# Kernel tuning notes

Hardware: AMD Instinct MI355X
Metric: run time of the kernel (lower is better)

Reference implementation:

```python
import jax, jax.numpy as jnp
import numpy as np

B, F, E = 16384, 50, 64

def setup_inputs() -> dict:
    key = jax.random.key(0)
    k1, k2, k3, k4 = jax.random.split(key, 4)
    g = jax.random.uniform(k1, (B, F, F), dtype=jnp.float32)
    h = jax.random.normal(k2, (B, F, E), dtype=jnp.float32)
    W_in = jax.random.normal(k3, (F, E, E), dtype=jnp.float32) * (2.0 / (E + E)) ** 0.5
    W_out = jax.random.normal(k4, (F, E, E), dtype=jnp.float32) * (2.0 / (E + E)) ** 0.5
    bias_p = jnp.zeros((E,), dtype=jnp.float32)
    return {"g": g, "h": h, "W_in": W_in, "W_out": W_out, "bias_p": bias_p}

def reference(g, h, W_in, W_out, bias_p):
    # per-field transform: [F,E,E] x [B,F,E] -> [B,F,E]
    h_out = jnp.einsum('fij,bfj->bfi', W_out, h)
    # graph aggregation over fields: [B,F,F] x [B,F,E] -> [B,F,E]
    aggr = jnp.einsum('bfg,bge->bfe', g, h_out)
    # per-field input transform + bias
    a = jnp.einsum('fij,bfj->bfi', W_in, aggr) + bias_p
    return a
```

## Files before the change

kernel.cpp:

```cpp
#include <hip/hip_runtime.h>


static constexpr int Bz  = 16384;
static constexpr int Ff  = 50;
static constexpr int Ee  = 64;
static constexpr int BT  = 128;
static constexpr int LDW = 68;

__device__ __forceinline__ void fma4(float4& a, float s, const float4& v) {
    a.x += s * v.x; a.y += s * v.y; a.z += s * v.z; a.w += s * v.w;
}

__global__ __launch_bounds__(128, 2)
void field_gemm(const float* __restrict__ src, float* __restrict__ dst,
                const float* __restrict__ W, const float* __restrict__ bias) {
    __shared__ float W_lds[Ee * LDW];
    __shared__ float h_lds[BT * LDW];
    const int f  = blockIdx.y;
    const int b0 = blockIdx.x * BT;
    const int t  = threadIdx.x;

    const float4* Wf4 = (const float4*)(W + f * Ee * Ee);
#pragma unroll
    for (int k = 0; k < 8; ++k) {
        int q = k * 128 + t;
        *(float4*)&W_lds[(q >> 4) * LDW + (q & 15) * 4] = Wf4[q];
    }
    const float4* s4 = (const float4*)src;
#pragma unroll
    for (int k = 0; k < 16; ++k) {
        int q = k * 128 + t;
        int r = q >> 4;
        *(float4*)&h_lds[r * LDW + (q & 15) * 4] =
            s4[(b0 + r) * (Ff * Ee / 4) + f * 16 + (q & 15)];
    }
    __syncthreads();

    const int ti = t & 7;
    const int tb = t >> 3;
    float acc[8][8];
#pragma unroll
    for (int ii = 0; ii < 8; ++ii)
#pragma unroll
        for (int kb = 0; kb < 8; ++kb) acc[ii][kb] = 0.f;

#pragma unroll 2
    for (int j0 = 0; j0 < Ee; j0 += 4) {
        float4 w4[8], h4[8];
#pragma unroll
        for (int ii = 0; ii < 8; ++ii)
            w4[ii] = *(const float4*)&W_lds[(ti + 8 * ii) * LDW + j0];
#pragma unroll
        for (int kb = 0; kb < 8; ++kb)
            h4[kb] = *(const float4*)&h_lds[(tb + 16 * kb) * LDW + j0];
#pragma unroll
        for (int ii = 0; ii < 8; ++ii)
#pragma unroll
            for (int kb = 0; kb < 8; ++kb) {
                acc[ii][kb] += w4[ii].x * h4[kb].x;
                acc[ii][kb] += w4[ii].y * h4[kb].y;
                acc[ii][kb] += w4[ii].z * h4[kb].z;
                acc[ii][kb] += w4[ii].w * h4[kb].w;
            }
    }

#pragma unroll
    for (int ii = 0; ii < 8; ++ii) {
        const int i  = ti + 8 * ii;
        const float bv = bias ? bias[i] : 0.0f;
#pragma unroll
        for (int kb = 0; kb < 8; ++kb) {
            const int bb = tb + 16 * kb;
            dst[(b0 + bb) * (Ff * Ee) + f * Ee + i] = acc[ii][kb] + bv;
        }
    }
}

static constexpr int HOP = 52 * Ee;
static constexpr int GPD = 2560;
static constexpr int WRG = HOP + GPD;

__global__ __launch_bounds__(128, 2)
void aggr_inplace(const float* __restrict__ g, float* __restrict__ ho) {
    __shared__ float lds[2 * WRG];
    const int t    = threadIdx.x;
    const int wid  = t >> 6;
    const int lane = t & 63;
    const int b    = blockIdx.x * 2 + wid;
    float* ho_sh = &lds[wid * WRG];
    float* g_sh  = ho_sh + HOP;

    const float4* hosrc = (const float4*)(ho + (size_t)b * (Ff * Ee));
    const float4* gsrc  = (const float4*)(g  + (size_t)b * (Ff * Ff));
#pragma unroll
    for (int k = 0; k < 13; ++k) {
        int q = k * 64 + lane;
        if (q < Ff * Ee / 4) *(float4*)&ho_sh[q * 4] = hosrc[q];
    }
#pragma unroll
    for (int k = 0; k < 10; ++k) {
        int q = k * 64 + lane;
        if (q < (Ff * Ff + 3) / 4) *(float4*)&g_sh[q * 4] = gsrc[q];
    }
    *(float2*)&ho_sh[Ff * Ee + lane * 2] = make_float2(0.f, 0.f);
    if (lane < 30) *(float2*)&g_sh[Ff * Ff + lane * 2] = make_float2(0.f, 0.f);
    __syncthreads();

    const int te = lane & 7;
    const int tf = lane >> 3;
    const int e0 = te * 8;
    float4 acc[7][2];
#pragma unroll
    for (int k = 0; k < 7; ++k) {
        acc[k][0] = make_float4(0.f, 0.f, 0.f, 0.f);
        acc[k][1] = make_float4(0.f, 0.f, 0.f, 0.f);
    }

#pragma unroll 2
    for (int g0 = 0; g0 < 52; g0 += 4) {
        float4 ho4[4][2];
#pragma unroll
        for (int q = 0; q < 4; ++q) {
            ho4[q][0] = *(const float4*)&ho_sh[(g0 + q) * Ee + e0];
            ho4[q][1] = *(const float4*)&ho_sh[(g0 + q) * Ee + e0 + 4];
        }
#pragma unroll
        for (int k = 0; k < 7; ++k) {
            int fi = tf * 7 + k;
            fi = (fi < Ff) ? fi : (Ff - 1);
            const float2 ga = *(const float2*)&g_sh[fi * Ff + g0];
            const float2 gb = *(const float2*)&g_sh[fi * Ff + g0 + 2];
            fma4(acc[k][0], ga.x, ho4[0][0]); fma4(acc[k][1], ga.x, ho4[0][1]);
            fma4(acc[k][0], ga.y, ho4[1][0]); fma4(acc[k][1], ga.y, ho4[1][1]);
            fma4(acc[k][0], gb.x, ho4[2][0]); fma4(acc[k][1], gb.x, ho4[2][1]);
            fma4(acc[k][0], gb.y, ho4[3][0]); fma4(acc[k][1], gb.y, ho4[3][1]);
        }
    }

    float* hb = ho + (size_t)b * (Ff * Ee);
#pragma unroll
    for (int k = 0; k < 7; ++k) {
        const int fi = tf * 7 + k;
        if (fi < Ff) {
            *(float4*)&hb[fi * Ee + e0]     = acc[k][0];
            *(float4*)&hb[fi * Ee + e0 + 4] = acc[k][1];
        }
    }
}

extern "C" void kernel_launch(void* const* d_in, const int* in_sizes, int n_in,
                              void* d_out, int out_size, void* d_ws, size_t ws_size,
                              hipStream_t stream) {
    const float* g     = (const float*)d_in[0];
    const float* h     = (const float*)d_in[1];
    const float* W_in  = (const float*)d_in[2];
    const float* W_out = (const float*)d_in[3];
    const float* bias  = (const float*)d_in[4];
    float* out = (float*)d_out;

    dim3 grid1(Bz / BT, Ff);
    field_gemm<<<grid1, 128, 0, stream>>>(h, out, W_out, nullptr);
    aggr_inplace<<<Bz / 2, 128, 0, stream>>>(g, out);
    field_gemm<<<grid1, 128, 0, stream>>>(out, out, W_in, bias);
}
```

Measured before the change: 674.8 us.

## Use direct global-to-LDS loads with XOR swizzle and larger batch tiles in field GEMM

The field GEMM kernel now loads W and h tiles with the global_load_lds builtin straight into shared memory, skipping the register staging. The padded layout is replaced by an XOR-swizzled unpadded one to avoid bank conflicts. The batch tile grows from 128 to 256 rows with 256 threads per block, which raises LDS use per block and may cost occupancy. The swizzle has to match exactly between the load path and the compute reads.

```diff
diff --git a/kernel.cpp b/kernel.cpp
--- a/kernel.cpp
+++ b/kernel.cpp
@@ -1,43 +1,55 @@
 #include <hip/hip_runtime.h>
+#include <stdint.h>
 
 
 static constexpr int Bz  = 16384;
 static constexpr int Ff  = 50;
 static constexpr int Ee  = 64;
-static constexpr int BT  = 128;
-static constexpr int LDW = 68;
+static constexpr int BT  = 256;
 
 __device__ __forceinline__ void fma4(float4& a, float s, const float4& v) {
     a.x += s * v.x; a.y += s * v.y; a.z += s * v.z; a.w += s * v.w;
 }
 
-__global__ __launch_bounds__(128, 2)
+__device__ __forceinline__ void gld_lds16(const float* gsrc, float* ldst) {
+    __builtin_amdgcn_global_load_lds(
+        (const __attribute__((address_space(1))) uint32_t*)gsrc,
+        (__attribute__((address_space(3))) uint32_t*)ldst, 16, 0, 0);
+}
+
+__global__ __launch_bounds__(256, 2)
 void field_gemm(const float* __restrict__ src, float* __restrict__ dst,
                 const float* __restrict__ W, const float* __restrict__ bias) {
-    __shared__ float W_lds[Ee * LDW];
-    __shared__ float h_lds[BT * LDW];
+    __shared__ float lds[Ee * Ee + BT * Ee];
+    float* W_lds = lds;
+    float* h_lds = lds + Ee * Ee;
     const int f  = blockIdx.y;
     const int b0 = blockIdx.x * BT;
     const int t  = threadIdx.x;
 
-    const float4* Wf4 = (const float4*)(W + f * Ee * Ee);
+    const float4* Wf4 = (const float4*)(W + f * (Ee * Ee));
 #pragma unroll
-    for (int k = 0; k < 8; ++k) {
-        int q = k * 128 + t;
-        *(float4*)&W_lds[(q >> 4) * LDW + (q & 15) * 4] = Wf4[q];
+    for (int k = 0; k < 4; ++k) {
+        int q = k * 256 + t;
+        int r = q >> 4, c = q & 15;
+        gld_lds16((const float*)&Wf4[r * 16 + (c ^ (r & 7))], &W_lds[q * 4]);
     }
     const float4* s4 = (const float4*)src;
 #pragma unroll
     for (int k = 0; k < 16; ++k) {
-        int q = k * 128 + t;
-        int r = q >> 4;
-        *(float4*)&h_lds[r * LDW + (q & 15) * 4] =
-            s4[(b0 + r) * (Ff * Ee / 4) + f * 16 + (q & 15)];
+        int q = k * 256 + t;
+        int r = q >> 4, c = q & 15;
+        gld_lds16((const float*)&s4[(b0 + r) * (Ff * Ee / 4) + f * 16 + (c ^ (r & 7))],
+                  &h_lds[q * 4]);
     }
     __syncthreads();
 
     const int ti = t & 7;
     const int tb = t >> 3;
+    const int tb7 = tb & 7;
+    const float4* wp = (const float4*)W_lds;
+    const float4* hp = (const float4*)h_lds;
+
     float acc[8][8];
 #pragma unroll
     for (int ii = 0; ii < 8; ++ii)
@@ -45,14 +57,14 @@
         for (int kb = 0; kb < 8; ++kb) acc[ii][kb] = 0.f;
 
 #pragma unroll 2
-    for (int j0 = 0; j0 < Ee; j0 += 4) {
+    for (int jq = 0; jq < 16; ++jq) {
         float4 w4[8], h4[8];
 #pragma unroll
         for (int ii = 0; ii < 8; ++ii)
-            w4[ii] = *(const float4*)&W_lds[(ti + 8 * ii) * LDW + j0];
+            w4[ii] = wp[(ti + 8 * ii) * 16 + (jq ^ ti)];
 #pragma unroll
         for (int kb = 0; kb < 8; ++kb)
-            h4[kb] = *(const float4*)&h_lds[(tb + 16 * kb) * LDW + j0];
+            h4[kb] = hp[(tb + 32 * kb) * 16 + (jq ^ tb7)];
 #pragma unroll
         for (int ii = 0; ii < 8; ++ii)
 #pragma unroll
@@ -70,7 +82,7 @@
         const float bv = bias ? bias[i] : 0.0f;
 #pragma unroll
         for (int kb = 0; kb < 8; ++kb) {
-            const int bb = tb + 16 * kb;
+            const int bb = tb + 32 * kb;
             dst[(b0 + bb) * (Ff * Ee) + f * Ee + i] = acc[ii][kb] + bv;
         }
     }
@@ -130,10 +142,10 @@
             fi = (fi < Ff) ? fi : (Ff - 1);
             const float2 ga = *(const float2*)&g_sh[fi * Ff + g0];
             const float2 gb = *(const float2*)&g_sh[fi * Ff + g0 + 2];
-            fma4(acc[k][0], ga.x, ho4[0][0]); fma4(acc[k][1], ga.x, ho4[0][1]);
-            fma4(acc[k][0], ga.y, ho4[1][0]); fma4(acc[k][1], ga.y, ho4[1][1]);
-            fma4(acc[k][0], gb.x, ho4[2][0]); fma4(acc[k][1], gb.x, ho4[2][1]);
-            fma4(acc[k][0], gb.y, ho4[3][0]); fma4(acc[k][1], gb.y, ho4[3][1]);
+            fma4(acc[k][0], ga.x,  ho4[0][0]); fma4(acc[k][1], ga.x,  ho4[0][1]);
+            fma4(acc[k][0], ga.y,  ho4[1][0]); fma4(acc[k][1], ga.y,  ho4[1][1]);
+            fma4(acc[k][0], gb.x,  ho4[2][0]); fma4(acc[k][1], gb.x,  ho4[2][1]);
+            fma4(acc[k][0], gb.y,  ho4[3][0]); fma4(acc[k][1], gb.y,  ho4[3][1]);
         }
     }
 
@@ -159,7 +171,7 @@
     float* out = (float*)d_out;
 
     dim3 grid1(Bz / BT, Ff);
-    field_gemm<<<grid1, 128, 0, stream>>>(h, out, W_out, nullptr);
+    field_gemm<<<grid1, 256, 0, stream>>>(h, out, W_out, nullptr);
     aggr_inplace<<<Bz / 2, 128, 0, stream>>>(g, out);
-    field_gemm<<<grid1, 128, 0, stream>>>(out, out, W_in, bias);
+    field_gemm<<<grid1, 256, 0, stream>>>(out, out, W_in, bias);
 }
```

New measurement: 653.9 us. 1.03x faster.

## Use direct global-to-LDS loads, read W and g from global, swizzle h tiles

Applied to the files above, without the earlier changes.

Both kernels now stage activations with global_load_lds (direct global-to-LDS DMA) instead of going through registers. In field_gemm the W tile is no longer staged in LDS but read straight from global/cache, and the h tile uses an XOR swizzle in place of padding to avoid bank conflicts. In aggr_inplace g is read directly from global memory instead of LDS, which cuts LDS use so three blocks fit per CU. The padded tail iteration is replaced by an explicit 2-field epilogue. This risks higher global-load latency in the inner loops for W and g, relying on L1/L2 hits.

```diff
diff --git a/kernel.cpp b/kernel.cpp
--- a/kernel.cpp
+++ b/kernel.cpp
@@ -1,43 +1,46 @@
 #include <hip/hip_runtime.h>
+#include <stdint.h>
 
 
 static constexpr int Bz  = 16384;
 static constexpr int Ff  = 50;
 static constexpr int Ee  = 64;
 static constexpr int BT  = 128;
-static constexpr int LDW = 68;
 
 __device__ __forceinline__ void fma4(float4& a, float s, const float4& v) {
     a.x += s * v.x; a.y += s * v.y; a.z += s * v.z; a.w += s * v.w;
 }
 
+__device__ __forceinline__ void gld_lds16(const float* gsrc, float* ldst) {
+    __builtin_amdgcn_global_load_lds(
+        (const __attribute__((address_space(1))) uint32_t*)gsrc,
+        (__attribute__((address_space(3))) uint32_t*)ldst, 16, 0, 0);
+}
+
 __global__ __launch_bounds__(128, 2)
 void field_gemm(const float* __restrict__ src, float* __restrict__ dst,
                 const float* __restrict__ W, const float* __restrict__ bias) {
-    __shared__ float W_lds[Ee * LDW];
-    __shared__ float h_lds[BT * LDW];
+    __shared__ __attribute__((aligned(16))) float h_lds[BT * Ee];
     const int f  = blockIdx.y;
     const int b0 = blockIdx.x * BT;
     const int t  = threadIdx.x;
 
-    const float4* Wf4 = (const float4*)(W + f * Ee * Ee);
-#pragma unroll
-    for (int k = 0; k < 8; ++k) {
-        int q = k * 128 + t;
-        *(float4*)&W_lds[(q >> 4) * LDW + (q & 15) * 4] = Wf4[q];
-    }
     const float4* s4 = (const float4*)src;
 #pragma unroll
     for (int k = 0; k < 16; ++k) {
         int q = k * 128 + t;
-        int r = q >> 4;
-        *(float4*)&h_lds[r * LDW + (q & 15) * 4] =
-            s4[(b0 + r) * (Ff * Ee / 4) + f * 16 + (q & 15)];
+        int r = q >> 4, c = q & 15;
+        gld_lds16((const float*)&s4[(size_t)(b0 + r) * (Ff * Ee / 4) + f * 16 + (c ^ (r & 7))],
+                  &h_lds[q * 4]);
     }
     __syncthreads();
 
-    const int ti = t & 7;
-    const int tb = t >> 3;
+    const int ti  = t & 7;
+    const int tb  = t >> 3;
+    const int tb7 = tb & 7;
+    const float4* hp = (const float4*)h_lds;
+    const float4* Wf = (const float4*)(W + (size_t)f * (Ee * Ee));
+
     float acc[8][8];
 #pragma unroll
     for (int ii = 0; ii < 8; ++ii)
@@ -45,14 +48,14 @@
         for (int kb = 0; kb < 8; ++kb) acc[ii][kb] = 0.f;
 
 #pragma unroll 2
-    for (int j0 = 0; j0 < Ee; j0 += 4) {
+    for (int jq = 0; jq < 16; ++jq) {
         float4 w4[8], h4[8];
 #pragma unroll
         for (int ii = 0; ii < 8; ++ii)
-            w4[ii] = *(const float4*)&W_lds[(ti + 8 * ii) * LDW + j0];
+            w4[ii] = Wf[(ti + 8 * ii) * 16 + jq];
 #pragma unroll
         for (int kb = 0; kb < 8; ++kb)
-            h4[kb] = *(const float4*)&h_lds[(tb + 16 * kb) * LDW + j0];
+            h4[kb] = hp[(tb + 16 * kb) * 16 + (jq ^ tb7)];
 #pragma unroll
         for (int ii = 0; ii < 8; ++ii)
 #pragma unroll
@@ -71,41 +74,35 @@
 #pragma unroll
         for (int kb = 0; kb < 8; ++kb) {
             const int bb = tb + 16 * kb;
-            dst[(b0 + bb) * (Ff * Ee) + f * Ee + i] = acc[ii][kb] + bv;
+            dst[(size_t)(b0 + bb) * (Ff * Ee) + f * Ee + i] = acc[ii][kb] + bv;
         }
     }
 }
 
-static constexpr int HOP = 52 * Ee;
-static constexpr int GPD = 2560;
-static constexpr int WRG = HOP + GPD;
+static constexpr int HOQ = (Ff * Ee) / 4;
 
-__global__ __launch_bounds__(128, 2)
+__global__ __launch_bounds__(128, 3)
 void aggr_inplace(const float* __restrict__ g, float* __restrict__ ho) {
-    __shared__ float lds[2 * WRG];
+    __shared__ __attribute__((aligned(16))) float lds[2 * HOQ * 4];
     const int t    = threadIdx.x;
     const int wid  = t >> 6;
     const int lane = t & 63;
     const int b    = blockIdx.x * 2 + wid;
-    float* ho_sh = &lds[wid * WRG];
-    float* g_sh  = ho_sh + HOP;
+    float* ho_sh = &lds[wid * (HOQ * 4)];
 
     const float4* hosrc = (const float4*)(ho + (size_t)b * (Ff * Ee));
-    const float4* gsrc  = (const float4*)(g  + (size_t)b * (Ff * Ff));
 #pragma unroll
-    for (int k = 0; k < 13; ++k) {
+    for (int k = 0; k < 12; ++k) {
         int q = k * 64 + lane;
-        if (q < Ff * Ee / 4) *(float4*)&ho_sh[q * 4] = hosrc[q];
+        gld_lds16((const float*)&hosrc[q], &ho_sh[q * 4]);
     }
-#pragma unroll
-    for (int k = 0; k < 10; ++k) {
-        int q = k * 64 + lane;
-        if (q < (Ff * Ff + 3) / 4) *(float4*)&g_sh[q * 4] = gsrc[q];
-    }
-    *(float2*)&ho_sh[Ff * Ee + lane * 2] = make_float2(0.f, 0.f);
-    if (lane < 30) *(float2*)&g_sh[Ff * Ff + lane * 2] = make_float2(0.f, 0.f);
-    __syncthreads();
+    if (lane < 32)
+        gld_lds16((const float*)&hosrc[768 + lane], &ho_sh[(768 + lane) * 4]);
 
+    asm volatile("s_waitcnt vmcnt(0)" ::: "memory");
+    __builtin_amdgcn_sched_barrier(0);
+
+    const float* gb = g + (size_t)b * (Ff * Ff);
     const int te = lane & 7;
     const int tf = lane >> 3;
     const int e0 = te * 8;
@@ -117,7 +114,7 @@
     }
 
 #pragma unroll 2
-    for (int g0 = 0; g0 < 52; g0 += 4) {
+    for (int g0 = 0; g0 < 48; g0 += 4) {
         float4 ho4[4][2];
 #pragma unroll
         for (int q = 0; q < 4; ++q) {
@@ -128,12 +125,27 @@
         for (int k = 0; k < 7; ++k) {
             int fi = tf * 7 + k;
             fi = (fi < Ff) ? fi : (Ff - 1);
-            const float2 ga = *(const float2*)&g_sh[fi * Ff + g0];
-            const float2 gb = *(const float2*)&g_sh[fi * Ff + g0 + 2];
+            const float2 ga = *(const float2*)&gb[fi * Ff + g0];
+            const float2 gc = *(const float2*)&gb[fi * Ff + g0 + 2];
             fma4(acc[k][0], ga.x, ho4[0][0]); fma4(acc[k][1], ga.x, ho4[0][1]);
             fma4(acc[k][0], ga.y, ho4[1][0]); fma4(acc[k][1], ga.y, ho4[1][1]);
-            fma4(acc[k][0], gb.x, ho4[2][0]); fma4(acc[k][1], gb.x, ho4[2][1]);
-            fma4(acc[k][0], gb.y, ho4[3][0]); fma4(acc[k][1], gb.y, ho4[3][1]);
+            fma4(acc[k][0], gc.x, ho4[2][0]); fma4(acc[k][1], gc.x, ho4[2][1]);
+            fma4(acc[k][0], gc.y, ho4[3][0]); fma4(acc[k][1], gc.y, ho4[3][1]);
+        }
+    }
+    {
+        float4 ho4[2][2];
+        ho4[0][0] = *(const float4*)&ho_sh[48 * Ee + e0];
+        ho4[0][1] = *(const float4*)&ho_sh[48 * Ee + e0 + 4];
+        ho4[1][0] = *(const float4*)&ho_sh[49 * Ee + e0];
+        ho4[1][1] = *(const float4*)&ho_sh[49 * Ee + e0 + 4];
+#pragma unroll
+        for (int k = 0; k < 7; ++k) {
+            int fi = tf * 7 + k;
+            fi = (fi < Ff) ? fi : (Ff - 1);
+            const float2 ga = *(const float2*)&gb[fi * Ff + 48];
+            fma4(acc[k][0], ga.x, ho4[0][0]); fma4(acc[k][1], ga.x, ho4[0][1]);
+            fma4(acc[k][0], ga.y, ho4[1][0]); fma4(acc[k][1], ga.y, ho4[1][1]);
         }
     }
 
```

Measured after the change: 1.024 ms. +51.7%, slower.
